# Kernel optimization log

Measured on AMD Instinct MI355X. Metric: run time of the kernel, lower is better.

Reference implementation:

```python
import jax, jax.numpy as jnp
import numpy as np

N, E, F, HID, HEADS, NC = 50000, 800000, 128, 32, 8, 10
SLOPE = 0.2  # PyG GATConv default negative_slope


def setup_inputs() -> dict:
    key = jax.random.key(0)
    ks = jax.random.split(key, 12)
    return {
        "x": jax.random.normal(ks[0], (N, F), jnp.float32),
        "edge_index": jax.random.randint(ks[1], (2, E), 0, N, jnp.int64),
        "W1": jax.random.normal(ks[2], (F, HEADS * HID), jnp.float32) * 0.05,
        "as1": jax.random.normal(ks[3], (HEADS, HID), jnp.float32) * 0.05,
        "ad1": jax.random.normal(ks[4], (HEADS, HID), jnp.float32) * 0.05,
        "b1": jnp.zeros((HEADS * HID,), jnp.float32),
        "W2": jax.random.normal(ks[5], (HEADS * HID, HID), jnp.float32) * 0.05,
        "as2": jax.random.normal(ks[6], (1, HID), jnp.float32) * 0.05,
        "ad2": jax.random.normal(ks[7], (1, HID), jnp.float32) * 0.05,
        "b2": jnp.zeros((HID,), jnp.float32),
        "Wl": jax.random.normal(ks[8], (HID, NC), jnp.float32) * 0.05,
        "bl": jnp.zeros((NC,), jnp.float32),
    }


def _gat_conv(x, src, dst, W, a_src, a_dst, b):
    # x: [N, Fin], W: [Fin, H*C], a_src/a_dst: [H, C]
    H, C = a_src.shape
    h = (x @ W).reshape(-1, H, C)                    # [N, H, C]
    alpha_s = jnp.einsum('nhc,hc->nh', h, a_src)      # [N, H]
    alpha_d = jnp.einsum('nhc,hc->nh', h, a_dst)      # [N, H]
    e = jax.nn.leaky_relu(alpha_s[src] + alpha_d[dst], SLOPE)  # [Etot, H]
    # segment softmax over incoming edges of each dst node
    m = jax.ops.segment_max(e, dst, num_segments=N)   # [N, H]
    ex = jnp.exp(e - m[dst])
    s = jax.ops.segment_sum(ex, dst, num_segments=N)  # [N, H]
    w = ex / (s[dst] + 1e-16)                         # [Etot, H]
    out = jax.ops.segment_sum(h[src] * w[:, :, None], dst, num_segments=N)  # [N, H, C]
    return out.reshape(-1, H * C) + b


def reference(x, edge_index, W1, as1, ad1, b1, W2, as2, ad2, b2, Wl, bl):
    # add self loops (PyG GATConv default add_self_loops=True)
    loops = jnp.arange(N, dtype=edge_index.dtype)
    src = jnp.concatenate([edge_index[0], loops])
    dst = jnp.concatenate([edge_index[1], loops])
    h = _gat_conv(x, src, dst, W1, as1, ad1, b1)   # [N, 8*32], concat heads
    h = jax.nn.elu(h)
    # dropout p=0.1 is a no-op in eval mode
    h = _gat_conv(h, src, dst, W2, as2, ad2, b2)   # [N, 32], single head
    h = jax.nn.elu(h)
    return h @ Wl + bl                              # [N, 10]
```

## Files before the change

### kernel.cpp

```cpp
#include <hip/hip_runtime.h>
#include <hip/hip_bf16.h>
#include <math.h>

#define N_NODES 50000
#define NEDGES  800000
#define ETOT    (NEDGES + N_NODES)
#define FIN     128
#define HID     32
#define HEADS   8
#define F1      (HEADS * HID)
#define NC      10
#define SLOPE   0.2f

__device__ __forceinline__ float leaky(float x) { return x > 0.f ? x : SLOPE * x; }
__device__ __forceinline__ float elu_f(float x) { return x > 0.f ? x : expm1f(x); }

__device__ __forceinline__ unsigned short f2bf(float f) {
    unsigned int u = __float_as_uint(f);
    u = (u + 0x7fffu + ((u >> 16) & 1u)) >> 16;
    return (unsigned short)u;
}
__device__ __forceinline__ float bflo(unsigned int u) {
    return __uint_as_float(u << 16);
}
__device__ __forceinline__ float bfhi(unsigned int u) {
    return __uint_as_float(u & 0xffff0000u);
}

__global__ void k_detect(const void* ei, int* flag) {
    const long long* p = (const long long*)ei;
    long long bad = 0;
#pragma unroll
    for (int i = 0; i < 8; ++i) {
        long long v = p[i];
        bad |= (v < 0 || v >= N_NODES) ? 1 : 0;
    }
    *flag = (bad == 0);
}

__device__ __forceinline__ int load_edge(const void* eiv, int is64, int idx) {
    if (is64) return (int)((const long long*)eiv)[idx];
    return ((const int*)eiv)[idx];
}

__global__ void k_deg(const void* eiv, const int* __restrict__ flag,
                      int* __restrict__ deg) {
    int i = blockIdx.x * blockDim.x + threadIdx.x;
    if (i >= ETOT) return;
    int d = (i < NEDGES) ? load_edge(eiv, *flag, NEDGES + i) : (i - NEDGES);
    atomicAdd(&deg[d], 1);
}

__global__ __launch_bounds__(1024) void k_scan(const int* __restrict__ deg,
                                               int* __restrict__ rowptr) {
    __shared__ int ssum[1024];
    __shared__ int s_carry;
    int tid = threadIdx.x;
    if (tid == 0) s_carry = 0;
    __syncthreads();
    const int PER  = 8;
    const int TILE = 1024 * PER;
    for (int base = 0; base < N_NODES; base += TILE) {
        int i0 = base + tid * PER;
        int v[PER];
        int tsum = 0;
#pragma unroll
        for (int k = 0; k < PER; ++k) {
            int i = i0 + k;
            v[k] = (i < N_NODES) ? deg[i] : 0;
            tsum += v[k];
        }
        ssum[tid] = tsum;
        __syncthreads();
        for (int off = 1; off < 1024; off <<= 1) {
            int t = (tid >= off) ? ssum[tid - off] : 0;
            __syncthreads();
            ssum[tid] += t;
            __syncthreads();
        }
        int excl = s_carry + ssum[tid] - tsum;
#pragma unroll
        for (int k = 0; k < PER; ++k) {
            int i = i0 + k;
            if (i < N_NODES) rowptr[i] = excl;
            excl += v[k];
        }
        __syncthreads();
        if (tid == 0) s_carry += ssum[1023];
        __syncthreads();
    }
    if (tid == 0) rowptr[N_NODES] = s_carry;
}

__global__ void k_fill(const void* eiv, const int* __restrict__ flag,
                       const int* __restrict__ rowptr, int* __restrict__ fill,
                       int* __restrict__ col) {
    int i = blockIdx.x * blockDim.x + threadIdx.x;
    if (i >= ETOT) return;
    int s, d;
    if (i < NEDGES) {
        int is64 = *flag;
        s = load_edge(eiv, is64, i);
        d = load_edge(eiv, is64, NEDGES + i);
    } else {
        s = i - NEDGES;
        d = s;
    }
    int pos = rowptr[d] + atomicAdd(&fill[d], 1);
    col[pos] = s;
}

__global__ __launch_bounds__(256) void k_gemm1(
    const float4* __restrict__ x4, const float* __restrict__ W1,
    const float* __restrict__ as1, const float* __restrict__ ad1,
    unsigned short* __restrict__ h1b, float* __restrict__ alpha_s,
    float* __restrict__ alpha_d) {
    __shared__ float xs[16][FIN];
    int tid = threadIdx.x;
    int node0 = blockIdx.x * 16;
    for (int idx = tid; idx < 16 * 32; idx += 256) {
        int m = idx >> 5, k4 = idx & 31;
        int n = node0 + m;
        float4 v = (n < N_NODES) ? x4[(size_t)n * 32 + k4] : float4{0.f, 0.f, 0.f, 0.f};
        *(float4*)&xs[m][k4 * 4] = v;
    }
    __syncthreads();
    float acc[16];
#pragma unroll
    for (int m = 0; m < 16; ++m) acc[m] = 0.f;
    for (int k = 0; k < FIN; k += 4) {
        float w0 = W1[(k + 0) * F1 + tid];
        float w1 = W1[(k + 1) * F1 + tid];
        float w2 = W1[(k + 2) * F1 + tid];
        float w3 = W1[(k + 3) * F1 + tid];
#pragma unroll
        for (int m = 0; m < 16; ++m) {
            float4 xv = *(const float4*)&xs[m][k];
            acc[m] = fmaf(xv.x, w0, acc[m]);
            acc[m] = fmaf(xv.y, w1, acc[m]);
            acc[m] = fmaf(xv.z, w2, acc[m]);
            acc[m] = fmaf(xv.w, w3, acc[m]);
        }
    }
    int head = tid >> 5, c = tid & 31;
    float a_s = as1[head * HID + c];
    float a_d = ad1[head * HID + c];
#pragma unroll
    for (int m = 0; m < 16; ++m) {
        int n = node0 + m;
        if (n >= N_NODES) break;
        h1b[(size_t)n * F1 + tid] = f2bf(acc[m]);
        float vs = acc[m] * a_s;
        float vd = acc[m] * a_d;
#pragma unroll
        for (int off = 16; off >= 1; off >>= 1) {
            vs += __shfl_xor(vs, off, 64);
            vd += __shfl_xor(vd, off, 64);
        }
        if (c == 0) {
            alpha_s[n * HEADS + head] = vs;
            alpha_d[n * HEADS + head] = vd;
        }
    }
}

__global__ __launch_bounds__(256) void k_agg1(
    const uint2* __restrict__ h1u, const float* __restrict__ a_s,
    const float* __restrict__ a_d, const int* __restrict__ rowptr,
    const int* __restrict__ col, const float4* __restrict__ b1,
    float4* __restrict__ hout) {
    int tid = threadIdx.x;
    int lane = tid & 63;
    int n = blockIdx.x * 4 + (tid >> 6);
    if (n >= N_NODES) return;
    int head = lane >> 3;
    int start = rowptr[n], end = rowptr[n + 1];
    float adv = a_d[n * HEADS + head];
    float4 acc = {0.f, 0.f, 0.f, 0.f};
    float ssum = 0.f;
    int j = start;
    for (; j + 3 < end; j += 4) {
        int s0 = col[j], s1 = col[j + 1], s2 = col[j + 2], s3 = col[j + 3];
        uint2 g0 = h1u[(size_t)s0 * 64 + lane];
        uint2 g1 = h1u[(size_t)s1 * 64 + lane];
        uint2 g2 = h1u[(size_t)s2 * 64 + lane];
        uint2 g3 = h1u[(size_t)s3 * 64 + lane];
        float w0 = expf(leaky(a_s[s0 * HEADS + head] + adv));
        float w1 = expf(leaky(a_s[s1 * HEADS + head] + adv));
        float w2 = expf(leaky(a_s[s2 * HEADS + head] + adv));
        float w3 = expf(leaky(a_s[s3 * HEADS + head] + adv));
        acc.x = fmaf(w0, bflo(g0.x), acc.x); acc.y = fmaf(w0, bfhi(g0.x), acc.y);
        acc.z = fmaf(w0, bflo(g0.y), acc.z); acc.w = fmaf(w0, bfhi(g0.y), acc.w);
        acc.x = fmaf(w1, bflo(g1.x), acc.x); acc.y = fmaf(w1, bfhi(g1.x), acc.y);
        acc.z = fmaf(w1, bflo(g1.y), acc.z); acc.w = fmaf(w1, bfhi(g1.y), acc.w);
        acc.x = fmaf(w2, bflo(g2.x), acc.x); acc.y = fmaf(w2, bfhi(g2.x), acc.y);
        acc.z = fmaf(w2, bflo(g2.y), acc.z); acc.w = fmaf(w2, bfhi(g2.y), acc.w);
        acc.x = fmaf(w3, bflo(g3.x), acc.x); acc.y = fmaf(w3, bfhi(g3.x), acc.y);
        acc.z = fmaf(w3, bflo(g3.y), acc.z); acc.w = fmaf(w3, bfhi(g3.y), acc.w);
        ssum += (w0 + w1) + (w2 + w3);
    }
    for (; j < end; ++j) {
        int s0 = col[j];
        uint2 g0 = h1u[(size_t)s0 * 64 + lane];
        float w0 = expf(leaky(a_s[s0 * HEADS + head] + adv));
        acc.x = fmaf(w0, bflo(g0.x), acc.x); acc.y = fmaf(w0, bfhi(g0.x), acc.y);
        acc.z = fmaf(w0, bflo(g0.y), acc.z); acc.w = fmaf(w0, bfhi(g0.y), acc.w);
        ssum += w0;
    }
    float inv = 1.f / ssum;
    float4 b = b1[lane];
    float4 o;
    o.x = elu_f(fmaf(acc.x, inv, b.x));
    o.y = elu_f(fmaf(acc.y, inv, b.y));
    o.z = elu_f(fmaf(acc.z, inv, b.z));
    o.w = elu_f(fmaf(acc.w, inv, b.w));
    hout[(size_t)n * 64 + lane] = o;
}

__global__ __launch_bounds__(256) void k_gemm2(
    const float4* __restrict__ hin4, const float* __restrict__ W2,
    const float* __restrict__ as2, const float* __restrict__ ad2,
    float* __restrict__ h2, float* __restrict__ alpha_s, float* __restrict__ alpha_d) {
    __shared__ float hs[16][F1];
    int tid = threadIdx.x;
    int node0 = blockIdx.x * 16;
    for (int idx = tid; idx < 16 * 64; idx += 256) {
        int m = idx >> 6, k4 = idx & 63;
        int n = node0 + m;
        float4 v = (n < N_NODES) ? hin4[(size_t)n * 64 + k4] : float4{0.f, 0.f, 0.f, 0.f};
        *(float4*)&hs[m][k4 * 4] = v;
    }
    __syncthreads();
    int m0 = tid >> 5, c = tid & 31;
    float accA = 0.f, accB = 0.f;
    for (int k = 0; k < F1; k += 4) {
        float w0 = W2[(k + 0) * HID + c];
        float w1 = W2[(k + 1) * HID + c];
        float w2 = W2[(k + 2) * HID + c];
        float w3 = W2[(k + 3) * HID + c];
        float4 xa = *(const float4*)&hs[m0][k];
        float4 xb = *(const float4*)&hs[m0 + 8][k];
        accA = fmaf(xa.w, w3, fmaf(xa.z, w2, fmaf(xa.y, w1, fmaf(xa.x, w0, accA))));
        accB = fmaf(xb.w, w3, fmaf(xb.z, w2, fmaf(xb.y, w1, fmaf(xb.x, w0, accB))));
    }
    float a_sc = as2[c];
    float a_dc = ad2[c];
#pragma unroll
    for (int half = 0; half < 2; ++half) {
        float acc = half ? accB : accA;
        int n = node0 + m0 + half * 8;
        if (n < N_NODES) {
            h2[(size_t)n * HID + c] = acc;
            float vs = acc * a_sc;
            float vd = acc * a_dc;
#pragma unroll
            for (int off = 16; off >= 1; off >>= 1) {
                vs += __shfl_xor(vs, off, 64);
                vd += __shfl_xor(vd, off, 64);
            }
            if (c == 0) {
                alpha_s[n] = vs;
                alpha_d[n] = vd;
            }
        }
    }
}

__global__ __launch_bounds__(256) void k_agg2(
    const float* __restrict__ h2, const float* __restrict__ a_s,
    const float* __restrict__ a_d, const int* __restrict__ rowptr,
    const int* __restrict__ col, const float* __restrict__ b2,
    float* __restrict__ hout) {
    int tid = threadIdx.x;
    int ml = tid >> 5, c = tid & 31;
    int n = blockIdx.x * 8 + ml;
    if (n >= N_NODES) return;
    int start = rowptr[n], end = rowptr[n + 1];
    float adv = a_d[n];
    float ssum = 0.f, acc = 0.f;
    int j = start;
    for (; j + 1 < end; j += 2) {
        int s0 = col[j], s1 = col[j + 1];
        float v0 = h2[(size_t)s0 * HID + c];
        float v1 = h2[(size_t)s1 * HID + c];
        float w0 = expf(leaky(a_s[s0] + adv));
        float w1 = expf(leaky(a_s[s1] + adv));
        acc = fmaf(w0, v0, acc);
        acc = fmaf(w1, v1, acc);
        ssum += w0 + w1;
    }
    if (j < end) {
        int s0 = col[j];
        float w0 = expf(leaky(a_s[s0] + adv));
        acc = fmaf(w0, h2[(size_t)s0 * HID + c], acc);
        ssum += w0;
    }
    hout[(size_t)n * HID + c] = elu_f(acc / ssum + b2[c]);
}

__global__ void k_final(const float* __restrict__ hf, const float* __restrict__ Wl,
                        const float* __restrict__ bl, float* __restrict__ out) {
    int n = blockIdx.x * blockDim.x + threadIdx.x;
    if (n >= N_NODES) return;
    float h[HID];
    const float4* hp = (const float4*)(hf + (size_t)n * HID);
#pragma unroll
    for (int i = 0; i < 8; ++i) {
        float4 v = hp[i];
        h[4 * i] = v.x; h[4 * i + 1] = v.y; h[4 * i + 2] = v.z; h[4 * i + 3] = v.w;
    }
#pragma unroll
    for (int j = 0; j < NC; ++j) {
        float acc = bl[j];
#pragma unroll
        for (int c = 0; c < HID; ++c) acc += h[c] * Wl[c * NC + j];
        out[(size_t)n * NC + j] = acc;
    }
}

extern "C" void kernel_launch(void* const* d_in, const int* in_sizes, int n_in,
                              void* d_out, int out_size, void* d_ws, size_t ws_size,
                              hipStream_t stream) {
    (void)in_sizes; (void)n_in; (void)out_size; (void)ws_size;
    const float* x   = (const float*)d_in[0];
    const void*  ei  = d_in[1];
    const float* W1  = (const float*)d_in[2];
    const float* as1 = (const float*)d_in[3];
    const float* ad1 = (const float*)d_in[4];
    const float* b1  = (const float*)d_in[5];
    const float* W2  = (const float*)d_in[6];
    const float* as2 = (const float*)d_in[7];
    const float* ad2 = (const float*)d_in[8];
    const float* b2  = (const float*)d_in[9];
    const float* Wl  = (const float*)d_in[10];
    const float* bl  = (const float*)d_in[11];
    float* out = (float*)d_out;

    char* ws = (char*)d_ws;
    size_t off = 0;
    auto alloc = [&](size_t bytes) {
        void* p = ws + off;
        off += (bytes + 255) & ~size_t(255);
        return p;
    };
    int*   flag    = (int*)alloc(4);
    int*   deg     = (int*)alloc(N_NODES * 4);
    int*   fill    = (int*)alloc(N_NODES * 4);
    int*   rowptr  = (int*)alloc((N_NODES + 1) * 4);
    int*   col     = (int*)alloc(ETOT * 4);
    unsigned short* h1b = (unsigned short*)alloc((size_t)N_NODES * F1 * 2);
    float* as1n    = (float*)alloc(N_NODES * HEADS * 4);
    float* ad1n    = (float*)alloc(N_NODES * HEADS * 4);
    float* hin2    = (float*)alloc((size_t)N_NODES * F1 * 4);
    float* h2      = (float*)alloc((size_t)N_NODES * HID * 4);
    float* as2n    = (float*)alloc(N_NODES * 4);
    float* ad2n    = (float*)alloc(N_NODES * 4);
    float* h2f     = (float*)h1b;

    hipMemsetAsync(deg, 0, N_NODES * 4, stream);
    hipMemsetAsync(fill, 0, N_NODES * 4, stream);

    k_detect<<<1, 1, 0, stream>>>(ei, flag);

    int egrid = (ETOT + 255) / 256;
    k_deg<<<egrid, 256, 0, stream>>>(ei, flag, deg);
    k_scan<<<1, 1024, 0, stream>>>(deg, rowptr);
    k_fill<<<egrid, 256, 0, stream>>>(ei, flag, rowptr, fill, col);

    int ngrid16 = (N_NODES + 15) / 16;
    k_gemm1<<<ngrid16, 256, 0, stream>>>((const float4*)x, W1, as1, ad1, h1b, as1n, ad1n);
    k_agg1<<<(N_NODES + 3) / 4, 256, 0, stream>>>((const uint2*)h1b, as1n, ad1n, rowptr,
                                                  col, (const float4*)b1, (float4*)hin2);
    k_gemm2<<<ngrid16, 256, 0, stream>>>((const float4*)hin2, W2, as2, ad2, h2, as2n, ad2n);
    k_agg2<<<(N_NODES + 7) / 8, 256, 0, stream>>>(h2, as2n, ad2n, rowptr, col, b2, h2f);
    k_final<<<(N_NODES + 255) / 256, 256, 0, stream>>>(h2f, Wl, bl, out);
}
```

Before: 428.2 us.

## Retile both node-transform GEMMs for more register reuse per thread

The first GEMM now processes 32 nodes per block, and each thread computes two output columns (c and c+128) for 16 nodes. This halves the weight reloads per node and increases the FMA work done per LDS read. The second GEMM now assigns one node row per 16 threads, each thread computing two columns, with the shared tile padded by 4 floats to reduce bank conflicts. The alpha reductions are adjusted to match the new layouts. The cost is more accumulator registers in gemm1, which may lower occupancy.

```diff
diff --git a/kernel.cpp b/kernel.cpp
--- a/kernel.cpp
+++ b/kernel.cpp
@@ -115,51 +115,67 @@
     const float* __restrict__ as1, const float* __restrict__ ad1,
     unsigned short* __restrict__ h1b, float* __restrict__ alpha_s,
     float* __restrict__ alpha_d) {
-    __shared__ float xs[16][FIN];
-    int tid = threadIdx.x;
-    int node0 = blockIdx.x * 16;
-    for (int idx = tid; idx < 16 * 32; idx += 256) {
+    __shared__ float xs[32][FIN];
+    int tid = threadIdx.x;
+    int node0 = blockIdx.x * 32;
+    for (int idx = tid; idx < 32 * 32; idx += 256) {
         int m = idx >> 5, k4 = idx & 31;
         int n = node0 + m;
         float4 v = (n < N_NODES) ? x4[(size_t)n * 32 + k4] : float4{0.f, 0.f, 0.f, 0.f};
         *(float4*)&xs[m][k4 * 4] = v;
     }
     __syncthreads();
-    float acc[16];
-#pragma unroll
-    for (int m = 0; m < 16; ++m) acc[m] = 0.f;
+    int c0 = tid & 127;
+    int mbase = (tid >> 7) * 16;
+    float accA[16], accB[16];
+#pragma unroll
+    for (int m = 0; m < 16; ++m) { accA[m] = 0.f; accB[m] = 0.f; }
     for (int k = 0; k < FIN; k += 4) {
-        float w0 = W1[(k + 0) * F1 + tid];
-        float w1 = W1[(k + 1) * F1 + tid];
-        float w2 = W1[(k + 2) * F1 + tid];
-        float w3 = W1[(k + 3) * F1 + tid];
+        float wa0 = W1[(k + 0) * F1 + c0];
+        float wa1 = W1[(k + 1) * F1 + c0];
+        float wa2 = W1[(k + 2) * F1 + c0];
+        float wa3 = W1[(k + 3) * F1 + c0];
+        float wb0 = W1[(k + 0) * F1 + c0 + 128];
+        float wb1 = W1[(k + 1) * F1 + c0 + 128];
+        float wb2 = W1[(k + 2) * F1 + c0 + 128];
+        float wb3 = W1[(k + 3) * F1 + c0 + 128];
 #pragma unroll
         for (int m = 0; m < 16; ++m) {
-            float4 xv = *(const float4*)&xs[m][k];
-            acc[m] = fmaf(xv.x, w0, acc[m]);
-            acc[m] = fmaf(xv.y, w1, acc[m]);
-            acc[m] = fmaf(xv.z, w2, acc[m]);
-            acc[m] = fmaf(xv.w, w3, acc[m]);
-        }
-    }
-    int head = tid >> 5, c = tid & 31;
-    float a_s = as1[head * HID + c];
-    float a_d = ad1[head * HID + c];
+            float4 xv = *(const float4*)&xs[mbase + m][k];
+            accA[m] = fmaf(xv.x, wa0, accA[m]);
+            accA[m] = fmaf(xv.y, wa1, accA[m]);
+            accA[m] = fmaf(xv.z, wa2, accA[m]);
+            accA[m] = fmaf(xv.w, wa3, accA[m]);
+            accB[m] = fmaf(xv.x, wb0, accB[m]);
+            accB[m] = fmaf(xv.y, wb1, accB[m]);
+            accB[m] = fmaf(xv.z, wb2, accB[m]);
+            accB[m] = fmaf(xv.w, wb3, accB[m]);
+        }
+    }
+    int headA = c0 >> 5, headB = headA + 4;
+    int cc = c0 & 31;
+    float aAs = as1[headA * HID + cc], aAd = ad1[headA * HID + cc];
+    float aBs = as1[headB * HID + cc], aBd = ad1[headB * HID + cc];
 #pragma unroll
     for (int m = 0; m < 16; ++m) {
-        int n = node0 + m;
+        int n = node0 + mbase + m;
         if (n >= N_NODES) break;
-        h1b[(size_t)n * F1 + tid] = f2bf(acc[m]);
-        float vs = acc[m] * a_s;
-        float vd = acc[m] * a_d;
+        h1b[(size_t)n * F1 + c0]       = f2bf(accA[m]);
+        h1b[(size_t)n * F1 + c0 + 128] = f2bf(accB[m]);
+        float vsA = accA[m] * aAs, vdA = accA[m] * aAd;
+        float vsB = accB[m] * aBs, vdB = accB[m] * aBd;
 #pragma unroll
         for (int off = 16; off >= 1; off >>= 1) {
-            vs += __shfl_xor(vs, off, 64);
-            vd += __shfl_xor(vd, off, 64);
-        }
-        if (c == 0) {
-            alpha_s[n * HEADS + head] = vs;
-            alpha_d[n * HEADS + head] = vd;
+            vsA += __shfl_xor(vsA, off, 64);
+            vdA += __shfl_xor(vdA, off, 64);
+            vsB += __shfl_xor(vsB, off, 64);
+            vdB += __shfl_xor(vdB, off, 64);
+        }
+        if (cc == 0) {
+            alpha_s[n * HEADS + headA] = vsA;
+            alpha_d[n * HEADS + headA] = vdA;
+            alpha_s[n * HEADS + headB] = vsB;
+            alpha_d[n * HEADS + headB] = vdB;
         }
     }
 }
@@ -221,7 +237,7 @@
     const float4* __restrict__ hin4, const float* __restrict__ W2,
     const float* __restrict__ as2, const float* __restrict__ ad2,
     float* __restrict__ h2, float* __restrict__ alpha_s, float* __restrict__ alpha_d) {
-    __shared__ float hs[16][F1];
+    __shared__ float hs[16][F1 + 4];
     int tid = threadIdx.x;
     int node0 = blockIdx.x * 16;
     for (int idx = tid; idx < 16 * 64; idx += 256) {
@@ -231,37 +247,36 @@
         *(float4*)&hs[m][k4 * 4] = v;
     }
     __syncthreads();
-    int m0 = tid >> 5, c = tid & 31;
-    float accA = 0.f, accB = 0.f;
+    int c = tid & 15;
+    int m = tid >> 4;
+    float acc0 = 0.f, acc1 = 0.f;
     for (int k = 0; k < F1; k += 4) {
-        float w0 = W2[(k + 0) * HID + c];
-        float w1 = W2[(k + 1) * HID + c];
-        float w2 = W2[(k + 2) * HID + c];
-        float w3 = W2[(k + 3) * HID + c];
-        float4 xa = *(const float4*)&hs[m0][k];
-        float4 xb = *(const float4*)&hs[m0 + 8][k];
-        accA = fmaf(xa.w, w3, fmaf(xa.z, w2, fmaf(xa.y, w1, fmaf(xa.x, w0, accA))));
-        accB = fmaf(xb.w, w3, fmaf(xb.z, w2, fmaf(xb.y, w1, fmaf(xb.x, w0, accB))));
-    }
-    float a_sc = as2[c];
-    float a_dc = ad2[c];
-#pragma unroll
-    for (int half = 0; half < 2; ++half) {
-        float acc = half ? accB : accA;
-        int n = node0 + m0 + half * 8;
-        if (n < N_NODES) {
-            h2[(size_t)n * HID + c] = acc;
-            float vs = acc * a_sc;
-            float vd = acc * a_dc;
-#pragma unroll
-            for (int off = 16; off >= 1; off >>= 1) {
-                vs += __shfl_xor(vs, off, 64);
-                vd += __shfl_xor(vd, off, 64);
-            }
-            if (c == 0) {
-                alpha_s[n] = vs;
-                alpha_d[n] = vd;
-            }
+        float w00 = W2[(k + 0) * HID + c];
+        float w01 = W2[(k + 1) * HID + c];
+        float w02 = W2[(k + 2) * HID + c];
+        float w03 = W2[(k + 3) * HID + c];
+        float w10 = W2[(k + 0) * HID + c + 16];
+        float w11 = W2[(k + 1) * HID + c + 16];
+        float w12 = W2[(k + 2) * HID + c + 16];
+        float w13 = W2[(k + 3) * HID + c + 16];
+        float4 xv = *(const float4*)&hs[m][k];
+        acc0 = fmaf(xv.w, w03, fmaf(xv.z, w02, fmaf(xv.y, w01, fmaf(xv.x, w00, acc0))));
+        acc1 = fmaf(xv.w, w13, fmaf(xv.z, w12, fmaf(xv.y, w11, fmaf(xv.x, w10, acc1))));
+    }
+    int n = node0 + m;
+    if (n < N_NODES) {
+        h2[(size_t)n * HID + c]      = acc0;
+        h2[(size_t)n * HID + c + 16] = acc1;
+        float vs = acc0 * as2[c] + acc1 * as2[c + 16];
+        float vd = acc0 * ad2[c] + acc1 * ad2[c + 16];
+#pragma unroll
+        for (int off = 8; off >= 1; off >>= 1) {
+            vs += __shfl_xor(vs, off, 64);
+            vd += __shfl_xor(vd, off, 64);
+        }
+        if (c == 0) {
+            alpha_s[n] = vs;
+            alpha_d[n] = vd;
         }
     }
 }
@@ -367,11 +382,12 @@
     k_scan<<<1, 1024, 0, stream>>>(deg, rowptr);
     k_fill<<<egrid, 256, 0, stream>>>(ei, flag, rowptr, fill, col);
 
-    int ngrid16 = (N_NODES + 15) / 16;
-    k_gemm1<<<ngrid16, 256, 0, stream>>>((const float4*)x, W1, as1, ad1, h1b, as1n, ad1n);
+    k_gemm1<<<(N_NODES + 31) / 32, 256, 0, stream>>>((const float4*)x, W1, as1, ad1,
+                                                     h1b, as1n, ad1n);
     k_agg1<<<(N_NODES + 3) / 4, 256, 0, stream>>>((const uint2*)h1b, as1n, ad1n, rowptr,
                                                   col, (const float4*)b1, (float4*)hin2);
-    k_gemm2<<<ngrid16, 256, 0, stream>>>((const float4*)hin2, W2, as2, ad2, h2, as2n, ad2n);
+    k_gemm2<<<(N_NODES + 15) / 16, 256, 0, stream>>>((const float4*)hin2, W2, as2, ad2,
+                                                     h2, as2n, ad2n);
     k_agg2<<<(N_NODES + 7) / 8, 256, 0, stream>>>(h2, as2n, ad2n, rowptr, col, b2, h2f);
     k_final<<<(N_NODES + 255) / 256, 256, 0, stream>>>(h2f, Wl, bl, out);
 }
```

After: 435.5 us. No clear change (+1.7%).
